# Optimization experiments

Measured on AMD Instinct MI355X. Metric: run time of the kernel, lower is better.

Reference implementation:

```python
import jax, jax.numpy as jnp
import numpy as np

B, T, D, H = 256, 512, 128, 256

def setup_inputs() -> dict:
    key = jax.random.key(0)
    ks = jax.random.split(key, 6)
    s = lambda n: 1.0 / np.sqrt(n)
    return {
        "x":  jax.random.normal(ks[0], (B, T, D), jnp.float32),
        "Wx": jax.random.normal(ks[1], (D, 4 * H), jnp.float32) * s(D),
        "Wh": jax.random.normal(ks[2], (H, 4 * H), jnp.float32) * s(H),
        "b":  jnp.zeros((4 * H,), jnp.float32),
        "W1": jax.random.normal(ks[3], (H, H), jnp.float32) * s(H),
        "b1": jnp.zeros((H,), jnp.float32),
        "W2": jax.random.normal(ks[4], (H, H), jnp.float32) * s(H),
        "b2": jnp.zeros((H,), jnp.float32),
        "W3": jax.random.normal(ks[5], (H, 1), jnp.float32) * s(H),
        "b3": jnp.zeros((1,), jnp.float32),
    }

def reference(x, Wx, Wh, b, W1, b1, W2, b2, W3, b3):
    # Precompute input projections for all timesteps: [B, T, 4H]
    xproj = jnp.einsum('btd,dg->btg', x, Wx) + b

    def step(carry, xp_t):
        h, c = carry
        gates = xp_t + h @ Wh  # [B, 4H]
        i, f, g, o = jnp.split(gates, 4, axis=-1)  # Keras order: i, f, c, o
        i = jax.nn.sigmoid(i)
        f = jax.nn.sigmoid(f)
        o = jax.nn.sigmoid(o)
        c_new = f * c + i * jnp.tanh(g)
        h_new = o * jnp.tanh(c_new)
        # per-step MLP head
        y = jnp.tanh(h_new @ W1 + b1)
        y = jnp.tanh(y @ W2 + b2)
        y = y @ W3 + b3  # [B, 1]
        return (h_new, c_new), y

    h0 = jnp.zeros((x.shape[0], Wh.shape[0]), x.dtype)
    c0 = jnp.zeros_like(h0)
    _, ys = jax.lax.scan(step, (h0, c0), jnp.swapaxes(xproj, 0, 1))  # ys: [T, B, 1]
    return jnp.swapaxes(ys, 0, 1)  # [B, T, 1]
```

## Files before the change

kernel.cpp:

```cpp
#include <hip/hip_runtime.h>

typedef _Float16 half8 __attribute__((ext_vector_type(8)));
typedef float f32x4 __attribute__((ext_vector_type(4)));

union H8U { unsigned long long u[2]; half8 v; unsigned short s[8]; };

__device__ __forceinline__ float fast_sigmoid(float v) {
  return 1.0f / (1.0f + __expf(-v));
}
__device__ __forceinline__ float fast_tanh(float v) {
  return 2.0f / (1.0f + __expf(-2.0f * v)) - 1.0f;
}

#define AL(p)    __hip_atomic_load((p), __ATOMIC_RELAXED, __HIP_MEMORY_SCOPE_AGENT)
#define AS(p, x) __hip_atomic_store((p), (x), __ATOMIC_RELAXED, __HIP_MEMORY_SCOPE_AGENT)
#define SWZ(i) ((i) ^ (((i) >> 6) & 7))

__global__ void __launch_bounds__(256) prep_kernel(
    const float* __restrict__ W1, const float* __restrict__ W2,
    _Float16* __restrict__ W1f, _Float16* __restrict__ W2f)
{
  int idx = blockIdx.x * 256 + threadIdx.x;
  int m  = idx >> 16;
  int i2 = idx & 65535;
  int s = i2 & 7, lane = (i2 >> 3) & 63, ks = (i2 >> 9) & 7, ct = (i2 >> 12) & 15;
  int col = ct * 16 + (lane & 15);
  int k   = ks * 32 + (lane >> 4) * 8 + s;
  float v = (m == 0) ? W1[k * 256 + col] : W2[k * 256 + col];
  _Float16* dst = (m == 0) ? W1f : W2f;
  dst[i2] = (_Float16)v;
}

__global__ void __launch_bounds__(256, 1) lstm_rec_kernel(
    const float* __restrict__ x, const float* __restrict__ Wx,
    const float* __restrict__ Wh, const float* __restrict__ bias,
    unsigned* __restrict__ hx, _Float16* __restrict__ h_all)
{
  __shared__ __align__(16) _Float16 Wt[8 * 12 * 64 * 8];
  __shared__ __align__(16) _Float16 At[2 * 12 * 64 * 8];

  const int tid = threadIdx.x;
  const int g  = blockIdx.x & 7;
  const int j  = blockIdx.x >> 3;
  const int b0 = g * 32;

  for (int idx = tid; idx < 384 * 128; idx += 256) {
    int k = idx >> 7, c = idx & 127;
    int q = c >> 5, d = c & 31;
    int gc = q * 256 + j * 32 + d;
    float v = (k < 128) ? Wx[k * 1024 + gc] : Wh[(k - 128) * 1024 + gc];
    int ct = c >> 4, lcol = c & 15;
    int ks = k >> 5, kg = (k >> 3) & 3, s = k & 7;
    Wt[(((ct * 12 + ks) * 64) + kg * 16 + lcol) * 8 + s] = (_Float16)v;
  }

  const int lane = tid & 63, wid = tid >> 6;
  const int rt = wid & 1, e = wid >> 1;
  const int prow = rt * 16 + ((lane >> 4) << 2);
  const int pc = lane & 15;
  const int gdim = j * 32 + e * 16 + pc;

  const float bv0 = bias[0 * 256 + gdim], bv1 = bias[1 * 256 + gdim],
              bv2 = bias[2 * 256 + gdim], bv3 = bias[3 * 256 + gdim];

  const int srow = tid >> 3, sseg = tid & 7;
  const int s_rt = srow >> 4, s_lrow = srow & 15;

  const float4* xb = (const float4*)x + (size_t)(b0 + srow) * 16384 + sseg * 4;
  float4 XR[4];
  XR[0] = xb[0]; XR[1] = xb[1]; XR[2] = xb[2]; XR[3] = xb[3];

  __syncthreads();

  half8 Bv[48];
  {
    const half8* Wp = (const half8*)Wt;
    #pragma unroll
    for (int q = 0; q < 4; ++q)
      #pragma unroll
      for (int ks = 0; ks < 12; ++ks)
        Bv[q * 12 + ks] = Wp[(2 * q + e) * 768 + ks * 64 + lane];
  }

  half8* Ag = (half8*)At;
  float cst[4] = {0.f, 0.f, 0.f, 0.f};
  f32x4 ax0, ax1, ax2, ax3;

  {
    half8 p0, p1;
    p0[0] = (_Float16)XR[0].x; p0[1] = (_Float16)XR[0].y;
    p0[2] = (_Float16)XR[0].z; p0[3] = (_Float16)XR[0].w;
    p0[4] = (_Float16)XR[1].x; p0[5] = (_Float16)XR[1].y;
    p0[6] = (_Float16)XR[1].z; p0[7] = (_Float16)XR[1].w;
    p1[0] = (_Float16)XR[2].x; p1[1] = (_Float16)XR[2].y;
    p1[2] = (_Float16)XR[2].z; p1[3] = (_Float16)XR[2].w;
    p1[4] = (_Float16)XR[3].x; p1[5] = (_Float16)XR[3].y;
    p1[6] = (_Float16)XR[3].z; p1[7] = (_Float16)XR[3].w;
    int xi = (s_rt * 12 + (sseg >> 1)) * 64 + ((sseg & 1) * 2) * 16 + s_lrow;
    Ag[SWZ(xi)] = p0; Ag[SWZ(xi + 16)] = p1;
  }
  __syncthreads();
  {
    ax0 = (f32x4){0.f, 0.f, 0.f, 0.f}; ax1 = ax0; ax2 = ax0; ax3 = ax0;
    #pragma unroll
    for (int ks = 0; ks < 4; ++ks) {
      half8 av = Ag[SWZ(rt * 768 + ks * 64 + lane)];
      ax0 = __builtin_amdgcn_mfma_f32_16x16x32_f16(av, Bv[0 * 12 + ks], ax0, 0, 0, 0);
      ax1 = __builtin_amdgcn_mfma_f32_16x16x32_f16(av, Bv[1 * 12 + ks], ax1, 0, 0, 0);
      ax2 = __builtin_amdgcn_mfma_f32_16x16x32_f16(av, Bv[2 * 12 + ks], ax2, 0, 0, 0);
      ax3 = __builtin_amdgcn_mfma_f32_16x16x32_f16(av, Bv[3 * 12 + ks], ax3, 0, 0, 0);
    }
  }
  XR[0] = xb[32]; XR[1] = xb[33]; XR[2] = xb[34]; XR[3] = xb[35];

  for (int t = 0; t < 512; ++t) {
    const int hbase = (s_rt * 12 + 4 + sseg) * 64 + s_lrow;
    if (t > 0) {
      const unsigned long long* hp = (const unsigned long long*)hx +
          (((t - 1) & 1) ? 32768 : 0) + (size_t)(b0 + srow) * 128 + sseg * 16;
      unsigned long long vv[16];
      const unsigned long long msk  = 0xFFFF0000FFFF0000ull;
      const unsigned long long want = ((unsigned long long)(unsigned)t << 16) |
                                      ((unsigned long long)(unsigned)t << 48);
      int iters = 0;
      while (true) {
        #pragma unroll
        for (int i = 0; i < 16; ++i) vv[i] = AL(hp + i);
        unsigned long long diff = 0;
        #pragma unroll
        for (int i = 0; i < 16; ++i) diff |= (vv[i] & msk) ^ want;
        if (diff == 0) break;
        if (++iters > (1 << 17)) break;
      }
      H8U pk[4];
      #pragma unroll
      for (int i = 0; i < 16; ++i) {
        pk[i >> 2].s[(2 * i) & 7]     = (unsigned short)vv[i];
        pk[i >> 2].s[(2 * i + 1) & 7] = (unsigned short)(vv[i] >> 32);
      }
      #pragma unroll
      for (int kg = 0; kg < 4; ++kg) Ag[SWZ(hbase + kg * 16)] = pk[kg].v;
    } else {
      H8U zz; zz.u[0] = 0ull; zz.u[1] = 0ull;
      #pragma unroll
      for (int kg = 0; kg < 4; ++kg) Ag[SWZ(hbase + kg * 16)] = zz.v;
    }
    __syncthreads();

    f32x4 a0 = ax0, a1 = ax1, a2 = ax2, a3 = ax3;
    #pragma unroll
    for (int ks = 4; ks < 12; ++ks) {
      half8 av = Ag[SWZ(rt * 768 + ks * 64 + lane)];
      a0 = __builtin_amdgcn_mfma_f32_16x16x32_f16(av, Bv[0 * 12 + ks], a0, 0, 0, 0);
      a1 = __builtin_amdgcn_mfma_f32_16x16x32_f16(av, Bv[1 * 12 + ks], a1, 0, 0, 0);
      a2 = __builtin_amdgcn_mfma_f32_16x16x32_f16(av, Bv[2 * 12 + ks], a2, 0, 0, 0);
      a3 = __builtin_amdgcn_mfma_f32_16x16x32_f16(av, Bv[3 * 12 + ks], a3, 0, 0, 0);
    }

    unsigned hw[4]; unsigned short hfb[4];
    #pragma unroll
    for (int r = 0; r < 4; ++r) {
      float iv = fast_sigmoid(a0[r] + bv0);
      float fv = fast_sigmoid(a1[r] + bv1);
      float gv = fast_tanh   (a2[r] + bv2);
      float ov = fast_sigmoid(a3[r] + bv3);
      cst[r] = fv * cst[r] + iv * gv;
      float hv = ov * fast_tanh(cst[r]);
      _Float16 hf = (_Float16)hv;
      unsigned short hb_; __builtin_memcpy(&hb_, &hf, 2);
      hfb[r] = hb_;
      hw[r] = ((unsigned)(t + 1) << 16) | (unsigned)hb_;
    }

    if (t < 511) {
      half8 p0, p1;
      p0[0] = (_Float16)XR[0].x; p0[1] = (_Float16)XR[0].y;
      p0[2] = (_Float16)XR[0].z; p0[3] = (_Float16)XR[0].w;
      p0[4] = (_Float16)XR[1].x; p0[5] = (_Float16)XR[1].y;
      p0[6] = (_Float16)XR[1].z; p0[7] = (_Float16)XR[1].w;
      p1[0] = (_Float16)XR[2].x; p1[1] = (_Float16)XR[2].y;
      p1[2] = (_Float16)XR[2].z; p1[3] = (_Float16)XR[2].w;
      p1[4] = (_Float16)XR[3].x; p1[5] = (_Float16)XR[3].y;
      p1[6] = (_Float16)XR[3].z; p1[7] = (_Float16)XR[3].w;
      int xi = (s_rt * 12 + (sseg >> 1)) * 64 + ((sseg & 1) * 2) * 16 + s_lrow;
      Ag[SWZ(xi)] = p0; Ag[SWZ(xi + 16)] = p1;
    }
    __syncthreads();

    {
      unsigned* hxp = hx + ((t & 1) ? 65536 : 0) + (size_t)(b0 + prow) * 256 + gdim;
      _Float16* hap = h_all + ((size_t)t * 256 + b0 + prow) * 256 + gdim;
      #pragma unroll
      for (int r = 0; r < 4; ++r) {
        AS(hxp + (size_t)r * 256, hw[r]);
        _Float16 hval; __builtin_memcpy(&hval, &hfb[r], 2);
        hap[(size_t)r * 256] = hval;
      }
    }

    if (t < 511) {
      ax0 = (f32x4){0.f, 0.f, 0.f, 0.f}; ax1 = ax0; ax2 = ax0; ax3 = ax0;
      #pragma unroll
      for (int ks = 0; ks < 4; ++ks) {
        half8 av = Ag[SWZ(rt * 768 + ks * 64 + lane)];
        ax0 = __builtin_amdgcn_mfma_f32_16x16x32_f16(av, Bv[0 * 12 + ks], ax0, 0, 0, 0);
        ax1 = __builtin_amdgcn_mfma_f32_16x16x32_f16(av, Bv[1 * 12 + ks], ax1, 0, 0, 0);
        ax2 = __builtin_amdgcn_mfma_f32_16x16x32_f16(av, Bv[2 * 12 + ks], ax2, 0, 0, 0);
        ax3 = __builtin_amdgcn_mfma_f32_16x16x32_f16(av, Bv[3 * 12 + ks], ax3, 0, 0, 0);
      }
      int tn = (t + 2 < 512) ? (t + 2) : 511;
      XR[0] = xb[(size_t)tn * 32 + 0]; XR[1] = xb[(size_t)tn * 32 + 1];
      XR[2] = xb[(size_t)tn * 32 + 2]; XR[3] = xb[(size_t)tn * 32 + 3];
    }
  }
}

__device__ __forceinline__ void head_gemm(const _Float16* __restrict__ A,
                                          const _Float16* __restrict__ Wf,
                                          const float* __restrict__ bvec,
                                          _Float16* __restrict__ Yd,
                                          int lane, int w)
{
  const half8* Af = (const half8*)A + w * 512 + lane;
  for (int ct = 0; ct < 16; ++ct) {
    const half8* Bf = (const half8*)Wf + ct * 512 + lane;
    f32x4 acc = {0.f, 0.f, 0.f, 0.f};
    #pragma unroll
    for (int ks = 0; ks < 8; ++ks)
      acc = __builtin_amdgcn_mfma_f32_16x16x32_f16(Af[ks * 64], Bf[ks * 64], acc, 0, 0, 0);
    int col = ct * 16 + (lane & 15);
    float bb = bvec[col];
    int ks2 = col >> 5, kg2 = (col >> 3) & 3, s2 = col & 7;
    #pragma unroll
    for (int r = 0; r < 4; ++r) {
      int row = w * 16 + ((lane >> 4) << 2) + r;
      float v = fast_tanh(acc[r] + bb);
      Yd[(((w * 8 + ks2) * 64) + kg2 * 16 + (row & 15)) * 8 + s2] = (_Float16)v;
    }
  }
}

__global__ void __launch_bounds__(256) head_kernel(
    const _Float16* __restrict__ h_all,
    const _Float16* __restrict__ W1f, const _Float16* __restrict__ W2f,
    const float* __restrict__ b1, const float* __restrict__ b2,
    const float* __restrict__ W3, const float* __restrict__ b3,
    float* __restrict__ out)
{
  __shared__ __align__(16) _Float16 A_s[16384];
  __shared__ __align__(16) _Float16 Y_s[16384];
  const int tid = threadIdx.x;
  const size_t r0 = (size_t)blockIdx.x * 64;

  {
    int row = tid >> 2, seg = tid & 3;
    int rtl = row >> 4, lrow = row & 15;
    const half8* hp = (const half8*)(h_all + (r0 + row) * 256 + seg * 64);
    #pragma unroll
    for (int i = 0; i < 8; ++i) {
      int k0 = seg * 64 + i * 8;
      int ks = k0 >> 5, kg = (k0 >> 3) & 3;
      ((half8*)A_s)[(rtl * 8 + ks) * 64 + kg * 16 + lrow] = hp[i];
    }
  }
  __syncthreads();

  const int lane = tid & 63, w = tid >> 6;
  head_gemm(A_s, W1f, b1, Y_s, lane, w);
  __syncthreads();
  head_gemm(Y_s, W2f, b2, A_s, lane, w);
  __syncthreads();

  {
    int row = tid >> 2, part = tid & 3;
    int rtl = row >> 4, lrow = row & 15;
    float p = 0.f;
    #pragma unroll
    for (int kk = 0; kk < 8; ++kk) {
      int k0 = part * 64 + kk * 8;
      int ks = k0 >> 5, kg = (k0 >> 3) & 3;
      half8 y = ((const half8*)A_s)[(rtl * 8 + ks) * 64 + kg * 16 + lrow];
      #pragma unroll
      for (int i = 0; i < 8; ++i) p += (float)y[i] * W3[k0 + i];
    }
    p += __shfl_xor(p, 1);
    p += __shfl_xor(p, 2);
    if (part == 0) {
      size_t r = r0 + row;
      int tt = (int)(r >> 8), bb = (int)(r & 255);
      out[(size_t)bb * 512 + tt] = p + b3[0];
    }
  }
}

extern "C" void kernel_launch(void* const* d_in, const int* in_sizes, int n_in,
                              void* d_out, int out_size, void* d_ws, size_t ws_size,
                              hipStream_t stream)
{
  const float* x  = (const float*)d_in[0];
  const float* Wx = (const float*)d_in[1];
  const float* Wh = (const float*)d_in[2];
  const float* b  = (const float*)d_in[3];
  const float* W1 = (const float*)d_in[4];
  const float* b1 = (const float*)d_in[5];
  const float* W2 = (const float*)d_in[6];
  const float* b2 = (const float*)d_in[7];
  const float* W3 = (const float*)d_in[8];
  const float* b3 = (const float*)d_in[9];
  float* out = (float*)d_out;

  char* ws = (char*)d_ws;
  unsigned*  hx    = (unsigned*)ws;
  _Float16*  W1f   = (_Float16*)(ws + 524288);
  _Float16*  W2f   = (_Float16*)(ws + 655360);
  _Float16*  h_all = (_Float16*)(ws + 786432);
  if (ws_size < (size_t)786432 + 67108864) return;

  hipMemsetAsync(hx, 0, 524288, stream);
  hipLaunchKernelGGL(prep_kernel, dim3(512), dim3(256), 0, stream,
                     W1, W2, W1f, W2f);
  hipLaunchKernelGGL(lstm_rec_kernel, dim3(64), dim3(256), 0, stream,
                     x, Wx, Wh, b, hx, h_all);
  hipLaunchKernelGGL(head_kernel, dim3(2048), dim3(256), 0, stream,
                     h_all, W1f, W2f, b1, b2, W3, b3, out);
}
```

Before: 2.172 ms.

## Halve recurrent blocks, sync via per-block flags, keep Wh in LDS

The recurrent kernel now runs on 32 blocks, each owning 64 hidden columns, instead of 64 blocks with 32 columns. The old scheme polled tagged 32-bit h values in a separate exchange buffer. Now each block stages h in LDS, writes f16 h straight into h_all, and publishes a release-ordered per-block step flag that consumers poll with a ballot and s_sleep. Wx is pre-swizzled to f16 by the prep kernel and held in registers, while Wh fragments are read from LDS each step instead of registers. The intent is fewer cross-block dependencies and less polling traffic per step. The cost is double the per-block MFMA work and LDS reads on the critical path.

```diff
diff --git a/kernel.cpp b/kernel.cpp
--- a/kernel.cpp
+++ b/kernel.cpp
@@ -2,8 +2,6 @@
 
 typedef _Float16 half8 __attribute__((ext_vector_type(8)));
 typedef float f32x4 __attribute__((ext_vector_type(4)));
-
-union H8U { unsigned long long u[2]; half8 v; unsigned short s[8]; };
 
 __device__ __forceinline__ float fast_sigmoid(float v) {
   return 1.0f / (1.0f + __expf(-v));
@@ -16,201 +14,206 @@
 #define AS(p, x) __hip_atomic_store((p), (x), __ATOMIC_RELAXED, __HIP_MEMORY_SCOPE_AGENT)
 #define SWZ(i) ((i) ^ (((i) >> 6) & 7))
 
+__device__ __forceinline__ half8 cvt2(float4 a, float4 b) {
+  half8 o;
+  o[0] = (_Float16)a.x; o[1] = (_Float16)a.y; o[2] = (_Float16)a.z; o[3] = (_Float16)a.w;
+  o[4] = (_Float16)b.x; o[5] = (_Float16)b.y; o[6] = (_Float16)b.z; o[7] = (_Float16)b.w;
+  return o;
+}
+
 __global__ void __launch_bounds__(256) prep_kernel(
     const float* __restrict__ W1, const float* __restrict__ W2,
-    _Float16* __restrict__ W1f, _Float16* __restrict__ W2f)
+    const float* __restrict__ Wx,
+    _Float16* __restrict__ W1f, _Float16* __restrict__ W2f,
+    _Float16* __restrict__ Wxf)
 {
   int idx = blockIdx.x * 256 + threadIdx.x;
-  int m  = idx >> 16;
-  int i2 = idx & 65535;
-  int s = i2 & 7, lane = (i2 >> 3) & 63, ks = (i2 >> 9) & 7, ct = (i2 >> 12) & 15;
-  int col = ct * 16 + (lane & 15);
-  int k   = ks * 32 + (lane >> 4) * 8 + s;
-  float v = (m == 0) ? W1[k * 256 + col] : W2[k * 256 + col];
-  _Float16* dst = (m == 0) ? W1f : W2f;
-  dst[i2] = (_Float16)v;
+  if (idx < 131072) {
+    int m  = idx >> 16;
+    int i2 = idx & 65535;
+    int s = i2 & 7, lane = (i2 >> 3) & 63, ks = (i2 >> 9) & 7, ct = (i2 >> 12) & 15;
+    int col = ct * 16 + (lane & 15);
+    int k   = ks * 32 + (lane >> 4) * 8 + s;
+    float v = (m == 0) ? W1[k * 256 + col] : W2[k * 256 + col];
+    _Float16* dst = (m == 0) ? W1f : W2f;
+    dst[i2] = (_Float16)v;
+  } else {
+    int wx = idx - 131072;
+    int s = wx & 7, lane = (wx >> 3) & 63, ks = (wx >> 9) & 3, gct = wx >> 11;
+    int col = gct * 16 + (lane & 15);
+    int k   = ks * 32 + (lane >> 4) * 8 + s;
+    Wxf[wx] = (_Float16)Wx[k * 1024 + col];
+  }
 }
 
 __global__ void __launch_bounds__(256, 1) lstm_rec_kernel(
-    const float* __restrict__ x, const float* __restrict__ Wx,
-    const float* __restrict__ Wh, const float* __restrict__ bias,
-    unsigned* __restrict__ hx, _Float16* __restrict__ h_all)
-{
-  __shared__ __align__(16) _Float16 Wt[8 * 12 * 64 * 8];
-  __shared__ __align__(16) _Float16 At[2 * 12 * 64 * 8];
+    const float* __restrict__ x, const float* __restrict__ Wh,
+    const float* __restrict__ bias, const _Float16* __restrict__ Wxf,
+    _Float16* __restrict__ h_all, unsigned* __restrict__ flags)
+{
+  __shared__ __align__(16) _Float16 Wt[16 * 8 * 64 * 8];
+  __shared__ __align__(16) _Float16 Ath[2 * 8 * 64 * 8];
+  __shared__ __align__(16) _Float16 h_s[32][72];
 
   const int tid = threadIdx.x;
   const int g  = blockIdx.x & 7;
   const int j  = blockIdx.x >> 3;
   const int b0 = g * 32;
 
-  for (int idx = tid; idx < 384 * 128; idx += 256) {
-    int k = idx >> 7, c = idx & 127;
-    int q = c >> 5, d = c & 31;
-    int gc = q * 256 + j * 32 + d;
-    float v = (k < 128) ? Wx[k * 1024 + gc] : Wh[(k - 128) * 1024 + gc];
-    int ct = c >> 4, lcol = c & 15;
+  for (int idx = tid; idx < 256 * 256; idx += 256) {
+    int k = idx >> 8, c = idx & 255;
+    int q = c >> 6, d = c & 63;
+    int gc = q * 256 + j * 64 + d;
+    int ct = q * 4 + (d >> 4), lcol = d & 15;
     int ks = k >> 5, kg = (k >> 3) & 3, s = k & 7;
-    Wt[(((ct * 12 + ks) * 64) + kg * 16 + lcol) * 8 + s] = (_Float16)v;
+    Wt[(((ct * 8 + ks) * 64) + kg * 16 + lcol) * 8 + s] = (_Float16)Wh[k * 1024 + gc];
   }
 
   const int lane = tid & 63, wid = tid >> 6;
   const int rt = wid & 1, e = wid >> 1;
+  const int pc = lane & 15;
   const int prow = rt * 16 + ((lane >> 4) << 2);
-  const int pc = lane & 15;
-  const int gdim = j * 32 + e * 16 + pc;
-
-  const float bv0 = bias[0 * 256 + gdim], bv1 = bias[1 * 256 + gdim],
-              bv2 = bias[2 * 256 + gdim], bv3 = bias[3 * 256 + gdim];
+  const int kg2 = (lane >> 4) * 2;
+
+  float bv[4][2];
+  #pragma unroll
+  for (int q = 0; q < 4; ++q)
+    #pragma unroll
+    for (int f = 0; f < 2; ++f)
+      bv[q][f] = bias[q * 256 + j * 64 + e * 32 + f * 16 + pc];
 
   const int srow = tid >> 3, sseg = tid & 7;
   const int s_rt = srow >> 4, s_lrow = srow & 15;
-
-  const float4* xb = (const float4*)x + (size_t)(b0 + srow) * 16384 + sseg * 4;
-  float4 XR[4];
-  XR[0] = xb[0]; XR[1] = xb[1]; XR[2] = xb[2]; XR[3] = xb[3];
+  const int hb = (s_rt * 8 + sseg) * 64 + s_lrow;
+
+  half8* Ath8 = (half8*)Ath;
+  const half8* Wp8 = (const half8*)Wt;
+
+  const float4* xl4 = (const float4*)x + (size_t)(b0 + rt * 16 + pc) * 16384;
 
   __syncthreads();
 
-  half8 Bv[48];
+  half8 Bx[4][2][4];
   {
-    const half8* Wp = (const half8*)Wt;
+    const half8* Wx8 = (const half8*)Wxf;
     #pragma unroll
     for (int q = 0; q < 4; ++q)
       #pragma unroll
-      for (int ks = 0; ks < 12; ++ks)
-        Bv[q * 12 + ks] = Wp[(2 * q + e) * 768 + ks * 64 + lane];
-  }
-
-  half8* Ag = (half8*)At;
-  float cst[4] = {0.f, 0.f, 0.f, 0.f};
-  f32x4 ax0, ax1, ax2, ax3;
-
-  {
-    half8 p0, p1;
-    p0[0] = (_Float16)XR[0].x; p0[1] = (_Float16)XR[0].y;
-    p0[2] = (_Float16)XR[0].z; p0[3] = (_Float16)XR[0].w;
-    p0[4] = (_Float16)XR[1].x; p0[5] = (_Float16)XR[1].y;
-    p0[6] = (_Float16)XR[1].z; p0[7] = (_Float16)XR[1].w;
-    p1[0] = (_Float16)XR[2].x; p1[1] = (_Float16)XR[2].y;
-    p1[2] = (_Float16)XR[2].z; p1[3] = (_Float16)XR[2].w;
-    p1[4] = (_Float16)XR[3].x; p1[5] = (_Float16)XR[3].y;
-    p1[6] = (_Float16)XR[3].z; p1[7] = (_Float16)XR[3].w;
-    int xi = (s_rt * 12 + (sseg >> 1)) * 64 + ((sseg & 1) * 2) * 16 + s_lrow;
-    Ag[SWZ(xi)] = p0; Ag[SWZ(xi + 16)] = p1;
-  }
-  __syncthreads();
-  {
-    ax0 = (f32x4){0.f, 0.f, 0.f, 0.f}; ax1 = ax0; ax2 = ax0; ax3 = ax0;
-    #pragma unroll
-    for (int ks = 0; ks < 4; ++ks) {
-      half8 av = Ag[SWZ(rt * 768 + ks * 64 + lane)];
-      ax0 = __builtin_amdgcn_mfma_f32_16x16x32_f16(av, Bv[0 * 12 + ks], ax0, 0, 0, 0);
-      ax1 = __builtin_amdgcn_mfma_f32_16x16x32_f16(av, Bv[1 * 12 + ks], ax1, 0, 0, 0);
-      ax2 = __builtin_amdgcn_mfma_f32_16x16x32_f16(av, Bv[2 * 12 + ks], ax2, 0, 0, 0);
-      ax3 = __builtin_amdgcn_mfma_f32_16x16x32_f16(av, Bv[3 * 12 + ks], ax3, 0, 0, 0);
-    }
-  }
-  XR[0] = xb[32]; XR[1] = xb[33]; XR[2] = xb[34]; XR[3] = xb[35];
+      for (int f = 0; f < 2; ++f) {
+        int gct = q * 16 + j * 4 + e * 2 + f;
+        #pragma unroll
+        for (int ks = 0; ks < 4; ++ks)
+          Bx[q][f][ks] = Wx8[(gct * 4 + ks) * 64 + lane];
+      }
+  }
+
+  half8 XF[4];
+  #pragma unroll
+  for (int ks = 0; ks < 4; ++ks)
+    XF[ks] = cvt2(xl4[ks * 8 + kg2], xl4[ks * 8 + kg2 + 1]);
+  f32x4 ac[4][2];
+  #pragma unroll
+  for (int q = 0; q < 4; ++q) {
+    ac[q][0] = (f32x4){0.f, 0.f, 0.f, 0.f};
+    ac[q][1] = (f32x4){0.f, 0.f, 0.f, 0.f};
+  }
+  #pragma unroll
+  for (int ks = 0; ks < 4; ++ks)
+    #pragma unroll
+    for (int q = 0; q < 4; ++q) {
+      ac[q][0] = __builtin_amdgcn_mfma_f32_16x16x32_f16(XF[ks], Bx[q][0][ks], ac[q][0], 0, 0, 0);
+      ac[q][1] = __builtin_amdgcn_mfma_f32_16x16x32_f16(XF[ks], Bx[q][1][ks], ac[q][1], 0, 0, 0);
+    }
+  #pragma unroll
+  for (int ks = 0; ks < 4; ++ks)
+    XF[ks] = cvt2(xl4[32 + ks * 8 + kg2], xl4[32 + ks * 8 + kg2 + 1]);
+
+  float cst[8];
+  #pragma unroll
+  for (int i = 0; i < 8; ++i) cst[i] = 0.f;
 
   for (int t = 0; t < 512; ++t) {
-    const int hbase = (s_rt * 12 + 4 + sseg) * 64 + s_lrow;
     if (t > 0) {
-      const unsigned long long* hp = (const unsigned long long*)hx +
-          (((t - 1) & 1) ? 32768 : 0) + (size_t)(b0 + srow) * 128 + sseg * 16;
-      unsigned long long vv[16];
-      const unsigned long long msk  = 0xFFFF0000FFFF0000ull;
-      const unsigned long long want = ((unsigned long long)(unsigned)t << 16) |
-                                      ((unsigned long long)(unsigned)t << 48);
       int iters = 0;
       while (true) {
+        unsigned v = (lane < 4) ? AL(&flags[g * 16 + lane]) : (unsigned)t;
+        if (__ballot(v >= (unsigned)t) == ~0ull) break;
+        if (++iters > (1 << 17)) break;
+        __builtin_amdgcn_s_sleep(1);
+      }
+      const unsigned long long* hp = (const unsigned long long*)h_all +
+          ((size_t)(t - 1) * 256 + b0 + srow) * 64 + sseg * 8;
+      union { unsigned long long u[2]; half8 v; } c0, c1, c2, c3;
+      c0.u[0] = AL(hp + 0); c0.u[1] = AL(hp + 1);
+      c1.u[0] = AL(hp + 2); c1.u[1] = AL(hp + 3);
+      c2.u[0] = AL(hp + 4); c2.u[1] = AL(hp + 5);
+      c3.u[0] = AL(hp + 6); c3.u[1] = AL(hp + 7);
+      Ath8[SWZ(hb)]      = c0.v; Ath8[SWZ(hb + 16)] = c1.v;
+      Ath8[SWZ(hb + 32)] = c2.v; Ath8[SWZ(hb + 48)] = c3.v;
+    } else {
+      half8 zz = {};
+      Ath8[SWZ(hb)]      = zz; Ath8[SWZ(hb + 16)] = zz;
+      Ath8[SWZ(hb + 32)] = zz; Ath8[SWZ(hb + 48)] = zz;
+    }
+    __syncthreads();
+
+    #pragma unroll
+    for (int ks = 0; ks < 8; ++ks) {
+      half8 av = Ath8[SWZ((rt * 8 + ks) * 64 + lane)];
+      #pragma unroll
+      for (int q = 0; q < 4; ++q) {
+        ac[q][0] = __builtin_amdgcn_mfma_f32_16x16x32_f16(
+            av, Wp8[((q * 4 + e * 2 + 0) * 8 + ks) * 64 + lane], ac[q][0], 0, 0, 0);
+        ac[q][1] = __builtin_amdgcn_mfma_f32_16x16x32_f16(
+            av, Wp8[((q * 4 + e * 2 + 1) * 8 + ks) * 64 + lane], ac[q][1], 0, 0, 0);
+      }
+    }
+
+    #pragma unroll
+    for (int f = 0; f < 2; ++f)
+      #pragma unroll
+      for (int r = 0; r < 4; ++r) {
+        float iv = fast_sigmoid(ac[0][f][r] + bv[0][f]);
+        float fv = fast_sigmoid(ac[1][f][r] + bv[1][f]);
+        float gv = fast_tanh   (ac[2][f][r] + bv[2][f]);
+        float ov = fast_sigmoid(ac[3][f][r] + bv[3][f]);
+        float cv = fv * cst[f * 4 + r] + iv * gv;
+        cst[f * 4 + r] = cv;
+        h_s[prow + r][e * 32 + f * 16 + pc] = (_Float16)(ov * fast_tanh(cv));
+      }
+    __syncthreads();
+
+    {
+      unsigned long long hv0, hv1;
+      __builtin_memcpy(&hv0, &h_s[srow][sseg * 8], 8);
+      __builtin_memcpy(&hv1, &h_s[srow][sseg * 8 + 4], 8);
+      unsigned long long* hp = (unsigned long long*)h_all +
+          ((size_t)t * 256 + b0 + srow) * 64 + j * 16 + sseg * 2;
+      AS(hp + 0, hv0); AS(hp + 1, hv1);
+    }
+    __syncthreads();
+    if (tid == 0)
+      __hip_atomic_store(&flags[g * 16 + j], (unsigned)(t + 1),
+                         __ATOMIC_RELEASE, __HIP_MEMORY_SCOPE_AGENT);
+
+    if (t < 511) {
+      #pragma unroll
+      for (int q = 0; q < 4; ++q) {
+        ac[q][0] = (f32x4){0.f, 0.f, 0.f, 0.f};
+        ac[q][1] = (f32x4){0.f, 0.f, 0.f, 0.f};
+      }
+      #pragma unroll
+      for (int ks = 0; ks < 4; ++ks)
         #pragma unroll
-        for (int i = 0; i < 16; ++i) vv[i] = AL(hp + i);
-        unsigned long long diff = 0;
-        #pragma unroll
-        for (int i = 0; i < 16; ++i) diff |= (vv[i] & msk) ^ want;
-        if (diff == 0) break;
-        if (++iters > (1 << 17)) break;
-      }
-      H8U pk[4];
-      #pragma unroll
-      for (int i = 0; i < 16; ++i) {
-        pk[i >> 2].s[(2 * i) & 7]     = (unsigned short)vv[i];
-        pk[i >> 2].s[(2 * i + 1) & 7] = (unsigned short)(vv[i] >> 32);
-      }
-      #pragma unroll
-      for (int kg = 0; kg < 4; ++kg) Ag[SWZ(hbase + kg * 16)] = pk[kg].v;
-    } else {
-      H8U zz; zz.u[0] = 0ull; zz.u[1] = 0ull;
-      #pragma unroll
-      for (int kg = 0; kg < 4; ++kg) Ag[SWZ(hbase + kg * 16)] = zz.v;
-    }
-    __syncthreads();
-
-    f32x4 a0 = ax0, a1 = ax1, a2 = ax2, a3 = ax3;
-    #pragma unroll
-    for (int ks = 4; ks < 12; ++ks) {
-      half8 av = Ag[SWZ(rt * 768 + ks * 64 + lane)];
-      a0 = __builtin_amdgcn_mfma_f32_16x16x32_f16(av, Bv[0 * 12 + ks], a0, 0, 0, 0);
-      a1 = __builtin_amdgcn_mfma_f32_16x16x32_f16(av, Bv[1 * 12 + ks], a1, 0, 0, 0);
-      a2 = __builtin_amdgcn_mfma_f32_16x16x32_f16(av, Bv[2 * 12 + ks], a2, 0, 0, 0);
-      a3 = __builtin_amdgcn_mfma_f32_16x16x32_f16(av, Bv[3 * 12 + ks], a3, 0, 0, 0);
-    }
-
-    unsigned hw[4]; unsigned short hfb[4];
-    #pragma unroll
-    for (int r = 0; r < 4; ++r) {
-      float iv = fast_sigmoid(a0[r] + bv0);
-      float fv = fast_sigmoid(a1[r] + bv1);
-      float gv = fast_tanh   (a2[r] + bv2);
-      float ov = fast_sigmoid(a3[r] + bv3);
-      cst[r] = fv * cst[r] + iv * gv;
-      float hv = ov * fast_tanh(cst[r]);
-      _Float16 hf = (_Float16)hv;
-      unsigned short hb_; __builtin_memcpy(&hb_, &hf, 2);
-      hfb[r] = hb_;
-      hw[r] = ((unsigned)(t + 1) << 16) | (unsigned)hb_;
-    }
-
-    if (t < 511) {
-      half8 p0, p1;
-      p0[0] = (_Float16)XR[0].x; p0[1] = (_Float16)XR[0].y;
-      p0[2] = (_Float16)XR[0].z; p0[3] = (_Float16)XR[0].w;
-      p0[4] = (_Float16)XR[1].x; p0[5] = (_Float16)XR[1].y;
-      p0[6] = (_Float16)XR[1].z; p0[7] = (_Float16)XR[1].w;
-      p1[0] = (_Float16)XR[2].x; p1[1] = (_Float16)XR[2].y;
-      p1[2] = (_Float16)XR[2].z; p1[3] = (_Float16)XR[2].w;
-      p1[4] = (_Float16)XR[3].x; p1[5] = (_Float16)XR[3].y;
-      p1[6] = (_Float16)XR[3].z; p1[7] = (_Float16)XR[3].w;
-      int xi = (s_rt * 12 + (sseg >> 1)) * 64 + ((sseg & 1) * 2) * 16 + s_lrow;
-      Ag[SWZ(xi)] = p0; Ag[SWZ(xi + 16)] = p1;
-    }
-    __syncthreads();
-
-    {
-      unsigned* hxp = hx + ((t & 1) ? 65536 : 0) + (size_t)(b0 + prow) * 256 + gdim;
-      _Float16* hap = h_all + ((size_t)t * 256 + b0 + prow) * 256 + gdim;
-      #pragma unroll
-      for (int r = 0; r < 4; ++r) {
-        AS(hxp + (size_t)r * 256, hw[r]);
-        _Float16 hval; __builtin_memcpy(&hval, &hfb[r], 2);
-        hap[(size_t)r * 256] = hval;
-      }
-    }
-
-    if (t < 511) {
-      ax0 = (f32x4){0.f, 0.f, 0.f, 0.f}; ax1 = ax0; ax2 = ax0; ax3 = ax0;
-      #pragma unroll
-      for (int ks = 0; ks < 4; ++ks) {
-        half8 av = Ag[SWZ(rt * 768 + ks * 64 + lane)];
-        ax0 = __builtin_amdgcn_mfma_f32_16x16x32_f16(av, Bv[0 * 12 + ks], ax0, 0, 0, 0);
-        ax1 = __builtin_amdgcn_mfma_f32_16x16x32_f16(av, Bv[1 * 12 + ks], ax1, 0, 0, 0);
-        ax2 = __builtin_amdgcn_mfma_f32_16x16x32_f16(av, Bv[2 * 12 + ks], ax2, 0, 0, 0);
-        ax3 = __builtin_amdgcn_mfma_f32_16x16x32_f16(av, Bv[3 * 12 + ks], ax3, 0, 0, 0);
-      }
+        for (int q = 0; q < 4; ++q) {
+          ac[q][0] = __builtin_amdgcn_mfma_f32_16x16x32_f16(XF[ks], Bx[q][0][ks], ac[q][0], 0, 0, 0);
+          ac[q][1] = __builtin_amdgcn_mfma_f32_16x16x32_f16(XF[ks], Bx[q][1][ks], ac[q][1], 0, 0, 0);
+        }
       int tn = (t + 2 < 512) ? (t + 2) : 511;
-      XR[0] = xb[(size_t)tn * 32 + 0]; XR[1] = xb[(size_t)tn * 32 + 1];
-      XR[2] = xb[(size_t)tn * 32 + 2]; XR[3] = xb[(size_t)tn * 32 + 3];
+      #pragma unroll
+      for (int ks = 0; ks < 4; ++ks)
+        XF[ks] = cvt2(xl4[(size_t)tn * 32 + ks * 8 + kg2],
+                      xl4[(size_t)tn * 32 + ks * 8 + kg2 + 1]);
     }
   }
 }
@@ -310,17 +313,18 @@
   float* out = (float*)d_out;
 
   char* ws = (char*)d_ws;
-  unsigned*  hx    = (unsigned*)ws;
-  _Float16*  W1f   = (_Float16*)(ws + 524288);
-  _Float16*  W2f   = (_Float16*)(ws + 655360);
-  _Float16*  h_all = (_Float16*)(ws + 786432);
-  if (ws_size < (size_t)786432 + 67108864) return;
-
-  hipMemsetAsync(hx, 0, 524288, stream);
-  hipLaunchKernelGGL(prep_kernel, dim3(512), dim3(256), 0, stream,
-                     W1, W2, W1f, W2f);
-  hipLaunchKernelGGL(lstm_rec_kernel, dim3(64), dim3(256), 0, stream,
-                     x, Wx, Wh, b, hx, h_all);
+  unsigned*  flags = (unsigned*)ws;
+  _Float16*  W1f   = (_Float16*)(ws + 4096);
+  _Float16*  W2f   = (_Float16*)(ws + 4096 + 131072);
+  _Float16*  Wxf   = (_Float16*)(ws + 4096 + 262144);
+  _Float16*  h_all = (_Float16*)(ws + 4096 + 524288);
+  if (ws_size < (size_t)4096 + 524288 + 67108864) return;
+
+  hipMemsetAsync(flags, 0, 4096, stream);
+  hipLaunchKernelGGL(prep_kernel, dim3(1024), dim3(256), 0, stream,
+                     W1, W2, Wx, W1f, W2f, Wxf);
+  hipLaunchKernelGGL(lstm_rec_kernel, dim3(32), dim3(256), 0, stream,
+                     x, Wh, b, Wxf, h_all, flags);
   hipLaunchKernelGGL(head_kernel, dim3(2048), dim3(256), 0, stream,
                      h_all, W1f, W2f, b1, b2, W3, b3, out);
 }
```

Result: slower. 3.067 ms (+41.2%).
